# Performance work log

Hardware: AMD Instinct MI355X
Metric: run time of the kernel (lower is better)

Reference implementation:

```python
import jax, jax.numpy as jnp
import numpy as np

B, T, D = 2, 2048, 1024
H = 16
DH = D // H            # 64, per-head dim
C = 128                # d_kv_compress
ROPE_BASE = 10000.0


def _rope_cos_sin(t_len, d_head, dtype):
    # freqs: (T, d_head/2); emb = cat(freqs, freqs) -> (T, d_head)
    inv_freq = 1.0 / (ROPE_BASE ** (jnp.arange(0, d_head, 2, dtype=jnp.float32) / d_head))
    freqs = jnp.arange(t_len, dtype=jnp.float32)[:, None] * inv_freq[None, :]
    emb = jnp.concatenate([freqs, freqs], axis=-1)
    return jnp.cos(emb).astype(dtype), jnp.sin(emb).astype(dtype)


def _rotate_half(x):
    x1, x2 = jnp.split(x, 2, axis=-1)
    return jnp.concatenate([-x2, x1], axis=-1)


def _apply_rope(x, cos, sin):
    # x: (B,H,T,DH); cos/sin: (T,DH)
    return x * cos[None, None] + _rotate_half(x) * sin[None, None]


def setup_inputs() -> dict:
    key = jax.random.key(0)
    ks = jax.random.split(key, 12)
    s = 0.02
    return {
        "x": jax.random.normal(ks[0], (B, T, D), dtype=jnp.float32),
        "w_dk": jax.random.normal(ks[1], (D, C), dtype=jnp.float32) * s,
        "b_dk": jnp.zeros((C,), dtype=jnp.float32),
        "w_dv": jax.random.normal(ks[2], (D, C), dtype=jnp.float32) * s,
        "b_dv": jnp.zeros((C,), dtype=jnp.float32),
        "w_uk": jax.random.normal(ks[3], (C, D), dtype=jnp.float32) * s,
        "b_uk": jnp.zeros((D,), dtype=jnp.float32),
        "w_uv": jax.random.normal(ks[4], (C, D), dtype=jnp.float32) * s,
        "b_uv": jnp.zeros((D,), dtype=jnp.float32),
        "w_o": jax.random.normal(ks[5], (D, D), dtype=jnp.float32) * s,
        "b_o": jnp.zeros((D,), dtype=jnp.float32),
    }


def reference(x, w_dk, b_dk, w_dv, b_dv, w_uk, b_uk, w_uv, b_uv, w_o, b_o):
    Bx, Tx, Dx = x.shape
    # low-rank KV compression then up-projection
    c_k = x @ w_dk + b_dk                      # (B,T,C)
    c_v = x @ w_dv + b_dv                      # (B,T,C)
    k = c_k @ w_uk + b_uk                      # (B,T,D)
    v = c_v @ w_uv + b_uv                      # (B,T,D)

    def split_heads(t):  # (B,T,D) -> (B,H,T,DH)
        return t.reshape(Bx, Tx, H, DH).transpose(0, 2, 1, 3)

    q = split_heads(x)
    k = split_heads(k)
    v = split_heads(v)

    cos, sin = _rope_cos_sin(Tx, DH, x.dtype)
    q = _apply_rope(q, cos, sin)
    k = _apply_rope(k, cos, sin)

    scale = 1.0 / np.sqrt(DH)
    attn = jnp.einsum('bhid,bhjd->bhij', q, k) * scale
    attn = jax.nn.softmax(attn, axis=-1)
    out = jnp.einsum('bhij,bhjd->bhid', attn, v)   # (B,H,T,DH)
    out = out.transpose(0, 2, 1, 3).reshape(Bx, Tx, Dx)
    return out @ w_o + b_o
```

## Files before the change

### kernel.cpp

```cpp
#include <hip/hip_runtime.h>
#include <hip/hip_bf16.h>
#include <math.h>

constexpr int kB  = 2;
constexpr int kT  = 2048;
constexpr int kD  = 1024;
constexpr int kH  = 16;
constexpr int kDH = 64;
constexpr int kC  = 128;
constexpr int kM  = kB * kT;
constexpr int kBH = kB * kH;

#define LOG10000_OVER_32 0.28782313662425575f
#define QSCALE 0.1803368801111773f

typedef unsigned short ushort_t;
using short8 = __attribute__((ext_vector_type(8))) short;
using f32x4  = __attribute__((ext_vector_type(4))) float;

__device__ inline ushort_t f2bf(float f) {
    __hip_bfloat16 h = __float2bfloat16(f);
    return *reinterpret_cast<ushort_t*>(&h);
}

__device__ inline short8 cvt8(const float* p) {
    float4 f0 = *reinterpret_cast<const float4*>(p);
    float4 f1 = *reinterpret_cast<const float4*>(p + 4);
    short8 v;
    v[0] = (short)f2bf(f0.x); v[1] = (short)f2bf(f0.y);
    v[2] = (short)f2bf(f0.z); v[3] = (short)f2bf(f0.w);
    v[4] = (short)f2bf(f1.x); v[5] = (short)f2bf(f1.y);
    v[6] = (short)f2bf(f1.z); v[7] = (short)f2bf(f1.w);
    return v;
}

__global__ __launch_bounds__(256)
void wtrans(const float* __restrict__ w_dk, const float* __restrict__ w_dv,
            const float* __restrict__ w_uk, const float* __restrict__ w_uv,
            const float* __restrict__ w_o,
            ushort_t* __restrict__ dkT, ushort_t* __restrict__ dvT,
            ushort_t* __restrict__ ukT, ushort_t* __restrict__ uvT,
            ushort_t* __restrict__ oT, float2* __restrict__ tab) {
    if (blockIdx.z == 5) {
        int flat = blockIdx.y * 32 + blockIdx.x;
        if (flat >= kT / 8) return;
        int t = flat * 8 + (threadIdx.x >> 5);
        int i = threadIdx.x & 31;
        float inv_freq = expf(-(float)i * LOG10000_OVER_32);
        float s, c;
        sincosf((float)t * inv_freq, &s, &c);
        tab[t * 32 + i] = make_float2(c, s);
        return;
    }
    const float* src; ushort_t* dst; int R, C;
    switch (blockIdx.z) {
        case 0: src = w_dk; dst = dkT; R = kD; C = kC; break;
        case 1: src = w_dv; dst = dvT; R = kD; C = kC; break;
        case 2: src = w_uk; dst = ukT; R = kC; C = kD; break;
        case 3: src = w_uv; dst = uvT; R = kC; C = kD; break;
        default: src = w_o; dst = oT;  R = kD; C = kD; break;
    }
    int c0 = blockIdx.x * 32, r0 = blockIdx.y * 32;
    if (c0 >= C || r0 >= R) return;

    __shared__ float Tl[32][33];
    int tx = threadIdx.x & 31, ty = threadIdx.x >> 5;
#pragma unroll
    for (int i = 0; i < 4; ++i)
        Tl[ty + 8 * i][tx] = src[(size_t)(r0 + ty + 8 * i) * C + c0 + tx];
    __syncthreads();
#pragma unroll
    for (int i = 0; i < 4; ++i)
        dst[(size_t)(c0 + ty + 8 * i) * R + r0 + tx] = f2bf(Tl[tx][ty + 8 * i]);
}

template<bool AF32, int MODE0, int MODE1>
__global__ __launch_bounds__(256)
void gemm_mfma(const void* __restrict__ A0_, const void* __restrict__ A1_,
               const ushort_t* __restrict__ Wt0, const float* __restrict__ bias0, void* __restrict__ C0,
               const ushort_t* __restrict__ Wt1, const float* __restrict__ bias1, void* __restrict__ C1,
               const float2* __restrict__ tab, int M, int N, int K) {
    constexpr int LDT = 40;
    __shared__ __align__(16) ushort_t As[128 * LDT];
    __shared__ __align__(16) ushort_t Bs[128 * LDT];

    const void*     A    = blockIdx.z ? A1_ : A0_;
    const ushort_t* Wt   = blockIdx.z ? Wt1 : Wt0;
    const float*    bias = blockIdx.z ? bias1 : bias0;
    void*           Cc   = blockIdx.z ? C1 : C0;
    const int       mode = blockIdx.z ? MODE1 : MODE0;

    const int tid  = threadIdx.x;
    const int wave = tid >> 6, lane = tid & 63;
    const int g = lane >> 4, cl = lane & 15;
    const int m0 = blockIdx.y * 128, n0 = blockIdx.x * 128;
    const int wm = (wave >> 1) * 64, wn = (wave & 1) * 64;

    const int ar = tid >> 1;
    const int ac = (tid & 1) * 16;

    f32x4 acc[4][4] = {};

    for (int k0 = 0; k0 < K; k0 += 32) {
        if constexpr (AF32) {
            const float* Af = (const float*)A + (size_t)(m0 + ar) * K + k0 + ac;
            *reinterpret_cast<short8*>(&As[ar * LDT + ac])     = cvt8(Af);
            *reinterpret_cast<short8*>(&As[ar * LDT + ac + 8]) = cvt8(Af + 8);
        } else {
            const ushort_t* Ab = (const ushort_t*)A + (size_t)(m0 + ar) * K + k0 + ac;
            *reinterpret_cast<short8*>(&As[ar * LDT + ac])     = *reinterpret_cast<const short8*>(Ab);
            *reinterpret_cast<short8*>(&As[ar * LDT + ac + 8]) = *reinterpret_cast<const short8*>(Ab + 8);
        }
        {
            const ushort_t* Wb = Wt + (size_t)(n0 + ar) * K + k0 + ac;
            *reinterpret_cast<short8*>(&Bs[ar * LDT + ac])     = *reinterpret_cast<const short8*>(Wb);
            *reinterpret_cast<short8*>(&Bs[ar * LDT + ac + 8]) = *reinterpret_cast<const short8*>(Wb + 8);
        }
        __syncthreads();

        short8 a[4], b[4];
#pragma unroll
        for (int mi = 0; mi < 4; ++mi)
            a[mi] = *reinterpret_cast<const short8*>(&As[(wm + mi * 16 + cl) * LDT + g * 8]);
#pragma unroll
        for (int ni = 0; ni < 4; ++ni)
            b[ni] = *reinterpret_cast<const short8*>(&Bs[(wn + ni * 16 + cl) * LDT + g * 8]);
#pragma unroll
        for (int mi = 0; mi < 4; ++mi)
#pragma unroll
            for (int ni = 0; ni < 4; ++ni)
                acc[mi][ni] = __builtin_amdgcn_mfma_f32_16x16x32_bf16(a[mi], b[ni], acc[mi][ni], 0, 0, 0);
        __syncthreads();
    }

#pragma unroll
    for (int mi = 0; mi < 4; ++mi) {
        if (mode == 4) {
            const int h = (n0 + wn) >> 6;
#pragma unroll
            for (int r = 0; r < 4; ++r) {
                const int m = m0 + wm + mi * 16 + 4 * g + r;
                const int bb = m >> 11, t = m & (kT - 1);
                ushort_t* kp = (ushort_t*)Cc + (((size_t)bb * kH + h) * kT + t) * kDH;
#pragma unroll
                for (int pr = 0; pr < 2; ++pr) {
                    const int i = pr * 16 + cl;
                    float2 cs = tab[t * 32 + i];
                    float v1 = acc[mi][pr][r]     + bias[n0 + wn + pr * 16 + cl];
                    float v2 = acc[mi][pr + 2][r] + bias[n0 + wn + (pr + 2) * 16 + cl];
                    kp[i]      = f2bf(v1 * cs.x - v2 * cs.y);
                    kp[i + 32] = f2bf(v2 * cs.x + v1 * cs.y);
                }
            }
            continue;
        }
#pragma unroll
        for (int ni = 0; ni < 4; ++ni) {
            const int mb = m0 + wm + mi * 16 + 4 * g;
            const int nn = n0 + wn + ni * 16 + cl;
            const float bv = bias[nn];
            if (mode == 0) {
#pragma unroll
                for (int r = 0; r < 4; ++r)
                    ((float*)Cc)[(size_t)(mb + r) * N + nn] = acc[mi][ni][r] + bv;
            } else if (mode == 3) {
#pragma unroll
                for (int r = 0; r < 4; ++r)
                    ((ushort_t*)Cc)[(size_t)(mb + r) * N + nn] = f2bf(acc[mi][ni][r] + bv);
            } else {
                const int h = nn >> 6, d = nn & (kDH - 1);
                const int bb = mb >> 11, t0 = mb & (kT - 1);
                uint2 u;
                u.x = (unsigned int)f2bf(acc[mi][ni][0] + bv) | ((unsigned int)f2bf(acc[mi][ni][1] + bv) << 16);
                u.y = (unsigned int)f2bf(acc[mi][ni][2] + bv) | ((unsigned int)f2bf(acc[mi][ni][3] + bv) << 16);
                ushort_t* vt = (ushort_t*)Cc;
                *reinterpret_cast<uint2*>(&vt[(((size_t)bb * kH + h) * kDH + d) * kT + t0]) = u;
            }
        }
    }
}

__global__ __launch_bounds__(256)
void rope_split_q(const float* __restrict__ x, const float2* __restrict__ tab,
                  ushort_t* __restrict__ q_bf) {
    int idx = blockIdx.x * 256 + threadIdx.x;
    int i = idx & 31;
    int h = (idx >> 5) & (kH - 1);
    int t = (idx >> 9) & (kT - 1);
    int b = idx >> 20;

    const float* xp = x + ((size_t)(b * kT + t)) * kD + h * kDH;
    float x1 = xp[i];
    float x2 = xp[i + 32];
    float2 cs = tab[t * 32 + i];

    ushort_t* qp = q_bf + (((size_t)(b * kH + h)) * kT + t) * kDH;
    qp[i]      = f2bf((x1 * cs.x - x2 * cs.y) * QSCALE);
    qp[i + 32] = f2bf((x2 * cs.x + x1 * cs.y) * QSCALE);
}

__global__ __launch_bounds__(256)
void attn_mfma(const ushort_t* __restrict__ q_bf, const ushort_t* __restrict__ k_bf,
               const ushort_t* __restrict__ vt_bf, ushort_t* __restrict__ att_bf) {
    constexpr int LDK = 72;
    constexpr int LDV = 40;
    constexpr int LDP = 36;
    const int blk  = blockIdx.x;
    const int bh   = (blk & 7) * 4 + ((blk >> 3) & 3);
    const int qt   = blk >> 5;
    const int tid  = threadIdx.x;
    const int wave = tid >> 6;
    const int lane = tid & 63;
    const int g = lane >> 4, c = lane & 15;
    const int qbase = qt * 128 + wave * 32;

    __shared__ __align__(16) ushort_t Ks[32 * LDK];
    __shared__ __align__(16) ushort_t Vs[64 * LDV];
    __shared__ __align__(16) ushort_t P_lds[4][32 * LDP];
    ushort_t* P = P_lds[wave];

    const ushort_t* qp = q_bf + ((size_t)bh * kT + qbase) * kDH;
    short8 qa[2][2];
#pragma unroll
    for (int qi = 0; qi < 2; ++qi)
#pragma unroll
        for (int f = 0; f < 2; ++f)
            qa[qi][f] = *reinterpret_cast<const short8*>(qp + (size_t)(qi * 16 + c) * kDH + f * 32 + g * 8);

    const ushort_t* kb = k_bf + (size_t)bh * kT * kDH;
    const ushort_t* vb = vt_bf + (size_t)bh * kDH * kT;

    const int kr_ = tid >> 3, kc_ = (tid & 7) * 8;
    const int vr_ = tid >> 2, vc_ = (tid & 3) * 8;

    f32x4 acc[2][4] = {};
    float lsum[2][4] = {};

    for (int kt = 0; kt < kT; kt += 32) {
        *reinterpret_cast<short8*>(&Ks[kr_ * LDK + kc_]) =
            *reinterpret_cast<const short8*>(&kb[(size_t)(kt + kr_) * kDH + kc_]);
        *reinterpret_cast<short8*>(&Vs[vr_ * LDV + vc_]) =
            *reinterpret_cast<const short8*>(&vb[(size_t)vr_ * kT + kt + vc_]);
        __syncthreads();

        short8 kf[2][2];
#pragma unroll
        for (int kj = 0; kj < 2; ++kj)
#pragma unroll
            for (int f = 0; f < 2; ++f)
                kf[kj][f] = *reinterpret_cast<const short8*>(&Ks[(kj * 16 + c) * LDK + f * 32 + g * 8]);

        f32x4 z = {0.f, 0.f, 0.f, 0.f};
        f32x4 s[2][2];
#pragma unroll
        for (int qi = 0; qi < 2; ++qi)
#pragma unroll
            for (int kj = 0; kj < 2; ++kj) {
                s[qi][kj] = __builtin_amdgcn_mfma_f32_16x16x32_bf16(qa[qi][0], kf[kj][0], z, 0, 0, 0);
                s[qi][kj] = __builtin_amdgcn_mfma_f32_16x16x32_bf16(qa[qi][1], kf[kj][1], s[qi][kj], 0, 0, 0);
            }

#pragma unroll
        for (int qi = 0; qi < 2; ++qi)
#pragma unroll
            for (int kj = 0; kj < 2; ++kj)
#pragma unroll
                for (int r = 0; r < 4; ++r) {
                    float p = exp2f(s[qi][kj][r]);
                    lsum[qi][r] += p;
                    P[(qi * 16 + 4 * g + r) * LDP + kj * 16 + c] = f2bf(p);
                }

        short8 pa[2];
#pragma unroll
        for (int qi = 0; qi < 2; ++qi)
            pa[qi] = *reinterpret_cast<const short8*>(&P[(qi * 16 + c) * LDP + g * 8]);

        short8 vf[4];
#pragma unroll
        for (int n = 0; n < 4; ++n)
            vf[n] = *reinterpret_cast<const short8*>(&Vs[(16 * n + c) * LDV + g * 8]);
#pragma unroll
        for (int qi = 0; qi < 2; ++qi)
#pragma unroll
            for (int n = 0; n < 4; ++n)
                acc[qi][n] = __builtin_amdgcn_mfma_f32_16x16x32_bf16(pa[qi], vf[n], acc[qi][n], 0, 0, 0);
        __syncthreads();
    }

#pragma unroll
    for (int off = 1; off < 16; off <<= 1)
#pragma unroll
        for (int qi = 0; qi < 2; ++qi)
#pragma unroll
            for (int r = 0; r < 4; ++r)
                lsum[qi][r] += __shfl_xor(lsum[qi][r], off, 64);

    const int b = bh >> 4, h = bh & (kH - 1);
#pragma unroll
    for (int qi = 0; qi < 2; ++qi)
#pragma unroll
        for (int r = 0; r < 4; ++r) {
            float inv_l = 1.0f / lsum[qi][r];
            size_t row = (size_t)(b * kT + qbase + qi * 16 + 4 * g + r) * kD + h * kDH;
#pragma unroll
            for (int n = 0; n < 4; ++n)
                att_bf[row + 16 * n + c] = f2bf(acc[qi][n][r] * inv_l);
        }
}

extern "C" void kernel_launch(void* const* d_in, const int* in_sizes, int n_in,
                              void* d_out, int out_size, void* d_ws, size_t ws_size,
                              hipStream_t stream) {
    const float* x    = (const float*)d_in[0];
    const float* w_dk = (const float*)d_in[1];
    const float* b_dk = (const float*)d_in[2];
    const float* w_dv = (const float*)d_in[3];
    const float* b_dv = (const float*)d_in[4];
    const float* w_uk = (const float*)d_in[5];
    const float* b_uk = (const float*)d_in[6];
    const float* w_uv = (const float*)d_in[7];
    const float* b_uv = (const float*)d_in[8];
    const float* w_o  = (const float*)d_in[9];
    const float* b_o  = (const float*)d_in[10];
    float* out = (float*)d_out;

    char* w = (char*)d_ws;
    ushort_t* q_bf   = (ushort_t*)w;  w += (size_t)kM * kD * 2;
    ushort_t* k_bf   = (ushort_t*)w;  w += (size_t)kM * kD * 2;
    ushort_t* vt_bf  = (ushort_t*)w;  w += (size_t)kM * kD * 2;
    ushort_t* att_bf = (ushort_t*)w;  w += (size_t)kM * kD * 2;
    ushort_t* ckbf   = (ushort_t*)w;  w += (size_t)kM * kC * 2;
    ushort_t* cvbf   = (ushort_t*)w;  w += (size_t)kM * kC * 2;
    ushort_t* dkT    = (ushort_t*)w;  w += (size_t)kC * kD * 2;
    ushort_t* dvT    = (ushort_t*)w;  w += (size_t)kC * kD * 2;
    ushort_t* ukT    = (ushort_t*)w;  w += (size_t)kD * kC * 2;
    ushort_t* uvT    = (ushort_t*)w;  w += (size_t)kD * kC * 2;
    ushort_t* oT     = (ushort_t*)w;  w += (size_t)kD * kD * 2;
    float2*   tab    = (float2*)w;    w += (size_t)kT * 32 * 8;

    dim3 blk(256);

    wtrans<<<dim3(32, 32, 6), blk, 0, stream>>>(w_dk, w_dv, w_uk, w_uv, w_o,
                                                dkT, dvT, ukT, uvT, oT, tab);

    gemm_mfma<true, 3, 3><<<dim3(kC / 128, kM / 128, 2), blk, 0, stream>>>(
        x, x, dkT, b_dk, ckbf, dvT, b_dv, cvbf, nullptr, kM, kC, kD);

    gemm_mfma<false, 4, 2><<<dim3(kD / 128, kM / 128, 2), blk, 0, stream>>>(
        ckbf, cvbf, ukT, b_uk, k_bf, uvT, b_uv, vt_bf, tab, kM, kD, kC);

    rope_split_q<<<(kB * kT * kH * 32) / 256, blk, 0, stream>>>(x, tab, q_bf);

    attn_mfma<<<dim3(kT / 128 * kBH), blk, 0, stream>>>(q_bf, k_bf, vt_bf, att_bf);

    gemm_mfma<false, 0, 0><<<dim3(kD / 128, kM / 128, 1), blk, 0, stream>>>(
        att_bf, att_bf, oT, b_o, out, oT, b_o, out, nullptr, kM, kD, kD);
}
```

Measured before the change: 266.0 us.

## Fuse Q RoPE into attention, double-buffer K/V, add 128x64 GEMM for small-N

Removes the separate rope_split_q kernel and q_bf buffer by computing rotated, scaled Q from x directly in the attention kernel. Attention now uses 16 query rows per wave with 64-row blocks, doubling grid size, and double-buffers K/V tiles in LDS with register prefetch so there is one barrier per step. A new 128x64-tile GEMM is used for the down-projection and output projection to raise block count. The up-projection GEMM is specialized to bf16 A only. Trade-off: less Q reuse per block and more K/V traffic per query.

```diff
diff --git a/kernel.cpp b/kernel.cpp
--- a/kernel.cpp
+++ b/kernel.cpp
@@ -74,9 +74,9 @@
         dst[(size_t)(c0 + ty + 8 * i) * R + r0 + tx] = f2bf(Tl[tx][ty + 8 * i]);
 }
 
-template<bool AF32, int MODE0, int MODE1>
+template<int MODE0, int MODE1>
 __global__ __launch_bounds__(256)
-void gemm_mfma(const void* __restrict__ A0_, const void* __restrict__ A1_,
+void gemm_mfma(const ushort_t* __restrict__ A0_, const ushort_t* __restrict__ A1_,
                const ushort_t* __restrict__ Wt0, const float* __restrict__ bias0, void* __restrict__ C0,
                const ushort_t* __restrict__ Wt1, const float* __restrict__ bias1, void* __restrict__ C1,
                const float2* __restrict__ tab, int M, int N, int K) {
@@ -84,7 +84,7 @@
     __shared__ __align__(16) ushort_t As[128 * LDT];
     __shared__ __align__(16) ushort_t Bs[128 * LDT];
 
-    const void*     A    = blockIdx.z ? A1_ : A0_;
+    const ushort_t* A    = blockIdx.z ? A1_ : A0_;
     const ushort_t* Wt   = blockIdx.z ? Wt1 : Wt0;
     const float*    bias = blockIdx.z ? bias1 : bias0;
     void*           Cc   = blockIdx.z ? C1 : C0;
@@ -100,6 +100,95 @@
     const int ac = (tid & 1) * 16;
 
     f32x4 acc[4][4] = {};
+
+    for (int k0 = 0; k0 < K; k0 += 32) {
+        {
+            const ushort_t* Ab = A + (size_t)(m0 + ar) * K + k0 + ac;
+            *reinterpret_cast<short8*>(&As[ar * LDT + ac])     = *reinterpret_cast<const short8*>(Ab);
+            *reinterpret_cast<short8*>(&As[ar * LDT + ac + 8]) = *reinterpret_cast<const short8*>(Ab + 8);
+            const ushort_t* Wb = Wt + (size_t)(n0 + ar) * K + k0 + ac;
+            *reinterpret_cast<short8*>(&Bs[ar * LDT + ac])     = *reinterpret_cast<const short8*>(Wb);
+            *reinterpret_cast<short8*>(&Bs[ar * LDT + ac + 8]) = *reinterpret_cast<const short8*>(Wb + 8);
+        }
+        __syncthreads();
+
+        short8 a[4], b[4];
+#pragma unroll
+        for (int mi = 0; mi < 4; ++mi)
+            a[mi] = *reinterpret_cast<const short8*>(&As[(wm + mi * 16 + cl) * LDT + g * 8]);
+#pragma unroll
+        for (int ni = 0; ni < 4; ++ni)
+            b[ni] = *reinterpret_cast<const short8*>(&Bs[(wn + ni * 16 + cl) * LDT + g * 8]);
+#pragma unroll
+        for (int mi = 0; mi < 4; ++mi)
+#pragma unroll
+            for (int ni = 0; ni < 4; ++ni)
+                acc[mi][ni] = __builtin_amdgcn_mfma_f32_16x16x32_bf16(a[mi], b[ni], acc[mi][ni], 0, 0, 0);
+        __syncthreads();
+    }
+
+#pragma unroll
+    for (int mi = 0; mi < 4; ++mi) {
+        if (mode == 4) {
+            const int h = (n0 + wn) >> 6;
+#pragma unroll
+            for (int r = 0; r < 4; ++r) {
+                const int m = m0 + wm + mi * 16 + 4 * g + r;
+                const int bb = m >> 11, t = m & (kT - 1);
+                ushort_t* kp = (ushort_t*)Cc + (((size_t)bb * kH + h) * kT + t) * kDH;
+#pragma unroll
+                for (int pr = 0; pr < 2; ++pr) {
+                    const int i = pr * 16 + cl;
+                    float2 cs = tab[t * 32 + i];
+                    float v1 = acc[mi][pr][r]     + bias[n0 + wn + pr * 16 + cl];
+                    float v2 = acc[mi][pr + 2][r] + bias[n0 + wn + (pr + 2) * 16 + cl];
+                    kp[i]      = f2bf(v1 * cs.x - v2 * cs.y);
+                    kp[i + 32] = f2bf(v2 * cs.x + v1 * cs.y);
+                }
+            }
+        } else {
+#pragma unroll
+            for (int ni = 0; ni < 4; ++ni) {
+                const int mb = m0 + wm + mi * 16 + 4 * g;
+                const int nn = n0 + wn + ni * 16 + cl;
+                const float bv = bias[nn];
+                const int h = nn >> 6, d = nn & (kDH - 1);
+                const int bb = mb >> 11, t0 = mb & (kT - 1);
+                uint2 u;
+                u.x = (unsigned int)f2bf(acc[mi][ni][0] + bv) | ((unsigned int)f2bf(acc[mi][ni][1] + bv) << 16);
+                u.y = (unsigned int)f2bf(acc[mi][ni][2] + bv) | ((unsigned int)f2bf(acc[mi][ni][3] + bv) << 16);
+                ushort_t* vt = (ushort_t*)Cc;
+                *reinterpret_cast<uint2*>(&vt[(((size_t)bb * kH + h) * kDH + d) * kT + t0]) = u;
+            }
+        }
+    }
+}
+
+template<bool AF32, int MODE>
+__global__ __launch_bounds__(256)
+void gemm64(const void* __restrict__ A0_, const void* __restrict__ A1_,
+            const ushort_t* __restrict__ Wt0, const float* __restrict__ bias0, void* __restrict__ C0,
+            const ushort_t* __restrict__ Wt1, const float* __restrict__ bias1, void* __restrict__ C1,
+            int M, int N, int K) {
+    constexpr int LDT = 40;
+    __shared__ __align__(16) ushort_t As[128 * LDT];
+    __shared__ __align__(16) ushort_t Bs[64 * LDT];
+
+    const void*     A    = blockIdx.z ? A1_ : A0_;
+    const ushort_t* Wt   = blockIdx.z ? Wt1 : Wt0;
+    const float*    bias = blockIdx.z ? bias1 : bias0;
+    void*           Cc   = blockIdx.z ? C1 : C0;
+
+    const int tid  = threadIdx.x;
+    const int wave = tid >> 6, lane = tid & 63;
+    const int g = lane >> 4, cl = lane & 15;
+    const int m0 = blockIdx.y * 128, n0 = blockIdx.x * 64;
+    const int wm = (wave >> 1) * 64, wn = (wave & 1) * 32;
+
+    const int ar = tid >> 1, ac = (tid & 1) * 16;
+    const int br = tid >> 2, bc = (tid & 3) * 8;
+
+    f32x4 acc[4][2] = {};
 
     for (int k0 = 0; k0 < K; k0 += 32) {
         if constexpr (AF32) {
@@ -111,97 +200,48 @@
             *reinterpret_cast<short8*>(&As[ar * LDT + ac])     = *reinterpret_cast<const short8*>(Ab);
             *reinterpret_cast<short8*>(&As[ar * LDT + ac + 8]) = *reinterpret_cast<const short8*>(Ab + 8);
         }
-        {
-            const ushort_t* Wb = Wt + (size_t)(n0 + ar) * K + k0 + ac;
-            *reinterpret_cast<short8*>(&Bs[ar * LDT + ac])     = *reinterpret_cast<const short8*>(Wb);
-            *reinterpret_cast<short8*>(&Bs[ar * LDT + ac + 8]) = *reinterpret_cast<const short8*>(Wb + 8);
-        }
+        *reinterpret_cast<short8*>(&Bs[br * LDT + bc]) =
+            *reinterpret_cast<const short8*>(Wt + (size_t)(n0 + br) * K + k0 + bc);
         __syncthreads();
 
-        short8 a[4], b[4];
+        short8 a[4], b[2];
 #pragma unroll
         for (int mi = 0; mi < 4; ++mi)
             a[mi] = *reinterpret_cast<const short8*>(&As[(wm + mi * 16 + cl) * LDT + g * 8]);
 #pragma unroll
-        for (int ni = 0; ni < 4; ++ni)
+        for (int ni = 0; ni < 2; ++ni)
             b[ni] = *reinterpret_cast<const short8*>(&Bs[(wn + ni * 16 + cl) * LDT + g * 8]);
 #pragma unroll
         for (int mi = 0; mi < 4; ++mi)
 #pragma unroll
-            for (int ni = 0; ni < 4; ++ni)
+            for (int ni = 0; ni < 2; ++ni)
                 acc[mi][ni] = __builtin_amdgcn_mfma_f32_16x16x32_bf16(a[mi], b[ni], acc[mi][ni], 0, 0, 0);
         __syncthreads();
     }
 
 #pragma unroll
-    for (int mi = 0; mi < 4; ++mi) {
-        if (mode == 4) {
-            const int h = (n0 + wn) >> 6;
-#pragma unroll
-            for (int r = 0; r < 4; ++r) {
-                const int m = m0 + wm + mi * 16 + 4 * g + r;
-                const int bb = m >> 11, t = m & (kT - 1);
-                ushort_t* kp = (ushort_t*)Cc + (((size_t)bb * kH + h) * kT + t) * kDH;
-#pragma unroll
-                for (int pr = 0; pr < 2; ++pr) {
-                    const int i = pr * 16 + cl;
-                    float2 cs = tab[t * 32 + i];
-                    float v1 = acc[mi][pr][r]     + bias[n0 + wn + pr * 16 + cl];
-                    float v2 = acc[mi][pr + 2][r] + bias[n0 + wn + (pr + 2) * 16 + cl];
-                    kp[i]      = f2bf(v1 * cs.x - v2 * cs.y);
-                    kp[i + 32] = f2bf(v2 * cs.x + v1 * cs.y);
-                }
-            }
-            continue;
-        }
-#pragma unroll
-        for (int ni = 0; ni < 4; ++ni) {
+    for (int mi = 0; mi < 4; ++mi)
+#pragma unroll
+        for (int ni = 0; ni < 2; ++ni) {
             const int mb = m0 + wm + mi * 16 + 4 * g;
             const int nn = n0 + wn + ni * 16 + cl;
             const float bv = bias[nn];
-            if (mode == 0) {
+            if constexpr (MODE == 0) {
 #pragma unroll
                 for (int r = 0; r < 4; ++r)
                     ((float*)Cc)[(size_t)(mb + r) * N + nn] = acc[mi][ni][r] + bv;
-            } else if (mode == 3) {
+            } else {
 #pragma unroll
                 for (int r = 0; r < 4; ++r)
                     ((ushort_t*)Cc)[(size_t)(mb + r) * N + nn] = f2bf(acc[mi][ni][r] + bv);
-            } else {
-                const int h = nn >> 6, d = nn & (kDH - 1);
-                const int bb = mb >> 11, t0 = mb & (kT - 1);
-                uint2 u;
-                u.x = (unsigned int)f2bf(acc[mi][ni][0] + bv) | ((unsigned int)f2bf(acc[mi][ni][1] + bv) << 16);
-                u.y = (unsigned int)f2bf(acc[mi][ni][2] + bv) | ((unsigned int)f2bf(acc[mi][ni][3] + bv) << 16);
-                ushort_t* vt = (ushort_t*)Cc;
-                *reinterpret_cast<uint2*>(&vt[(((size_t)bb * kH + h) * kDH + d) * kT + t0]) = u;
             }
         }
-    }
 }
 
 __global__ __launch_bounds__(256)
-void rope_split_q(const float* __restrict__ x, const float2* __restrict__ tab,
-                  ushort_t* __restrict__ q_bf) {
-    int idx = blockIdx.x * 256 + threadIdx.x;
-    int i = idx & 31;
-    int h = (idx >> 5) & (kH - 1);
-    int t = (idx >> 9) & (kT - 1);
-    int b = idx >> 20;
-
-    const float* xp = x + ((size_t)(b * kT + t)) * kD + h * kDH;
-    float x1 = xp[i];
-    float x2 = xp[i + 32];
-    float2 cs = tab[t * 32 + i];
-
-    ushort_t* qp = q_bf + (((size_t)(b * kH + h)) * kT + t) * kDH;
-    qp[i]      = f2bf((x1 * cs.x - x2 * cs.y) * QSCALE);
-    qp[i + 32] = f2bf((x2 * cs.x + x1 * cs.y) * QSCALE);
-}
-
-__global__ __launch_bounds__(256)
-void attn_mfma(const ushort_t* __restrict__ q_bf, const ushort_t* __restrict__ k_bf,
-               const ushort_t* __restrict__ vt_bf, ushort_t* __restrict__ att_bf) {
+void attn_mfma(const float* __restrict__ x, const float2* __restrict__ tab,
+               const ushort_t* __restrict__ k_bf, const ushort_t* __restrict__ vt_bf,
+               ushort_t* __restrict__ att_bf) {
     constexpr int LDK = 72;
     constexpr int LDV = 40;
     constexpr int LDP = 36;
@@ -209,23 +249,35 @@
     const int bh   = (blk & 7) * 4 + ((blk >> 3) & 3);
     const int qt   = blk >> 5;
     const int tid  = threadIdx.x;
-    const int wave = tid >> 6;
-    const int lane = tid & 63;
+    const int wave = tid >> 6, lane = tid & 63;
     const int g = lane >> 4, c = lane & 15;
-    const int qbase = qt * 128 + wave * 32;
-
-    __shared__ __align__(16) ushort_t Ks[32 * LDK];
-    __shared__ __align__(16) ushort_t Vs[64 * LDV];
-    __shared__ __align__(16) ushort_t P_lds[4][32 * LDP];
+    const int qbase = qt * 64 + wave * 16;
+    const int b = bh >> 4, h = bh & (kH - 1);
+
+    __shared__ __align__(16) ushort_t Ks[2][32 * LDK];
+    __shared__ __align__(16) ushort_t Vs[2][64 * LDV];
+    __shared__ __align__(16) ushort_t P_lds[4][16 * LDP];
     ushort_t* P = P_lds[wave];
 
-    const ushort_t* qp = q_bf + ((size_t)bh * kT + qbase) * kDH;
-    short8 qa[2][2];
-#pragma unroll
-    for (int qi = 0; qi < 2; ++qi)
-#pragma unroll
-        for (int f = 0; f < 2; ++f)
-            qa[qi][f] = *reinterpret_cast<const short8*>(qp + (size_t)(qi * 16 + c) * kDH + f * 32 + g * 8);
+    short8 qa0, qa1;
+    {
+        const int t = qbase + c;
+        const float* xp = x + ((size_t)(b * kT + t)) * kD + h * kDH + g * 8;
+        float xa[8], xb[8]; float2 cs[8];
+        *reinterpret_cast<float4*>(&xa[0]) = *reinterpret_cast<const float4*>(xp);
+        *reinterpret_cast<float4*>(&xa[4]) = *reinterpret_cast<const float4*>(xp + 4);
+        *reinterpret_cast<float4*>(&xb[0]) = *reinterpret_cast<const float4*>(xp + 32);
+        *reinterpret_cast<float4*>(&xb[4]) = *reinterpret_cast<const float4*>(xp + 36);
+        const float2* tp = tab + (size_t)t * 32 + g * 8;
+#pragma unroll
+        for (int j = 0; j < 8; j += 2)
+            *reinterpret_cast<float4*>(&cs[j]) = *reinterpret_cast<const float4*>(tp + j);
+#pragma unroll
+        for (int j = 0; j < 8; ++j) {
+            qa0[j] = (short)f2bf((xa[j] * cs[j].x - xb[j] * cs[j].y) * QSCALE);
+            qa1[j] = (short)f2bf((xb[j] * cs[j].x + xa[j] * cs[j].y) * QSCALE);
+        }
+    }
 
     const ushort_t* kb = k_bf + (size_t)bh * kT * kDH;
     const ushort_t* vb = vt_bf + (size_t)bh * kDH * kT;
@@ -233,80 +285,78 @@
     const int kr_ = tid >> 3, kc_ = (tid & 7) * 8;
     const int vr_ = tid >> 2, vc_ = (tid & 3) * 8;
 
-    f32x4 acc[2][4] = {};
-    float lsum[2][4] = {};
+    {
+        short8 kreg = *reinterpret_cast<const short8*>(&kb[(size_t)kr_ * kDH + kc_]);
+        short8 vreg = *reinterpret_cast<const short8*>(&vb[(size_t)vr_ * kT + vc_]);
+        *reinterpret_cast<short8*>(&Ks[0][kr_ * LDK + kc_]) = kreg;
+        *reinterpret_cast<short8*>(&Vs[0][vr_ * LDV + vc_]) = vreg;
+    }
+    __syncthreads();
+
+    f32x4 acc[4] = {};
+    float lsum[4] = {};
 
     for (int kt = 0; kt < kT; kt += 32) {
-        *reinterpret_cast<short8*>(&Ks[kr_ * LDK + kc_]) =
-            *reinterpret_cast<const short8*>(&kb[(size_t)(kt + kr_) * kDH + kc_]);
-        *reinterpret_cast<short8*>(&Vs[vr_ * LDV + vc_]) =
-            *reinterpret_cast<const short8*>(&vb[(size_t)vr_ * kT + kt + vc_]);
+        const int cur = (kt >> 5) & 1;
+        short8 kreg, vreg;
+        const bool more = (kt + 32) < kT;
+        if (more) {
+            kreg = *reinterpret_cast<const short8*>(&kb[(size_t)(kt + 32 + kr_) * kDH + kc_]);
+            vreg = *reinterpret_cast<const short8*>(&vb[(size_t)vr_ * kT + kt + 32 + vc_]);
+        }
+
+        short8 kf[2][2];
+#pragma unroll
+        for (int kj = 0; kj < 2; ++kj)
+#pragma unroll
+            for (int f = 0; f < 2; ++f)
+                kf[kj][f] = *reinterpret_cast<const short8*>(&Ks[cur][(kj * 16 + c) * LDK + f * 32 + g * 8]);
+
+        f32x4 z = {0.f, 0.f, 0.f, 0.f};
+        f32x4 s0 = __builtin_amdgcn_mfma_f32_16x16x32_bf16(qa0, kf[0][0], z, 0, 0, 0);
+        s0 = __builtin_amdgcn_mfma_f32_16x16x32_bf16(qa1, kf[0][1], s0, 0, 0, 0);
+        f32x4 s1 = __builtin_amdgcn_mfma_f32_16x16x32_bf16(qa0, kf[1][0], z, 0, 0, 0);
+        s1 = __builtin_amdgcn_mfma_f32_16x16x32_bf16(qa1, kf[1][1], s1, 0, 0, 0);
+
+#pragma unroll
+        for (int r = 0; r < 4; ++r) {
+            float p0 = exp2f(s0[r]);
+            float p1 = exp2f(s1[r]);
+            lsum[r] += p0 + p1;
+            P[(4 * g + r) * LDP + c]      = f2bf(p0);
+            P[(4 * g + r) * LDP + 16 + c] = f2bf(p1);
+        }
+        short8 pa = *reinterpret_cast<const short8*>(&P[c * LDP + g * 8]);
+
+        short8 vf[4];
+#pragma unroll
+        for (int n = 0; n < 4; ++n)
+            vf[n] = *reinterpret_cast<const short8*>(&Vs[cur][(16 * n + c) * LDV + g * 8]);
+#pragma unroll
+        for (int n = 0; n < 4; ++n)
+            acc[n] = __builtin_amdgcn_mfma_f32_16x16x32_bf16(pa, vf[n], acc[n], 0, 0, 0);
+
+        if (more) {
+            *reinterpret_cast<short8*>(&Ks[cur ^ 1][kr_ * LDK + kc_]) = kreg;
+            *reinterpret_cast<short8*>(&Vs[cur ^ 1][vr_ * LDV + vc_]) = vreg;
+        }
         __syncthreads();
-
-        short8 kf[2][2];
-#pragma unroll
-        for (int kj = 0; kj < 2; ++kj)
-#pragma unroll
-            for (int f = 0; f < 2; ++f)
-                kf[kj][f] = *reinterpret_cast<const short8*>(&Ks[(kj * 16 + c) * LDK + f * 32 + g * 8]);
-
-        f32x4 z = {0.f, 0.f, 0.f, 0.f};
-        f32x4 s[2][2];
-#pragma unroll
-        for (int qi = 0; qi < 2; ++qi)
-#pragma unroll
-            for (int kj = 0; kj < 2; ++kj) {
-                s[qi][kj] = __builtin_amdgcn_mfma_f32_16x16x32_bf16(qa[qi][0], kf[kj][0], z, 0, 0, 0);
-                s[qi][kj] = __builtin_amdgcn_mfma_f32_16x16x32_bf16(qa[qi][1], kf[kj][1], s[qi][kj], 0, 0, 0);
-            }
-
-#pragma unroll
-        for (int qi = 0; qi < 2; ++qi)
-#pragma unroll
-            for (int kj = 0; kj < 2; ++kj)
-#pragma unroll
-                for (int r = 0; r < 4; ++r) {
-                    float p = exp2f(s[qi][kj][r]);
-                    lsum[qi][r] += p;
-                    P[(qi * 16 + 4 * g + r) * LDP + kj * 16 + c] = f2bf(p);
-                }
-
-        short8 pa[2];
-#pragma unroll
-        for (int qi = 0; qi < 2; ++qi)
-            pa[qi] = *reinterpret_cast<const short8*>(&P[(qi * 16 + c) * LDP + g * 8]);
-
-        short8 vf[4];
+    }
+
+#pragma unroll
+    for (int off = 1; off < 16; off <<= 1)
+#pragma unroll
+        for (int r = 0; r < 4; ++r)
+            lsum[r] += __shfl_xor(lsum[r], off, 64);
+
+#pragma unroll
+    for (int r = 0; r < 4; ++r) {
+        float inv_l = 1.0f / lsum[r];
+        size_t row = (size_t)(b * kT + qbase + 4 * g + r) * kD + h * kDH;
 #pragma unroll
         for (int n = 0; n < 4; ++n)
-            vf[n] = *reinterpret_cast<const short8*>(&Vs[(16 * n + c) * LDV + g * 8]);
-#pragma unroll
-        for (int qi = 0; qi < 2; ++qi)
-#pragma unroll
-            for (int n = 0; n < 4; ++n)
-                acc[qi][n] = __builtin_amdgcn_mfma_f32_16x16x32_bf16(pa[qi], vf[n], acc[qi][n], 0, 0, 0);
-        __syncthreads();
-    }
-
-#pragma unroll
-    for (int off = 1; off < 16; off <<= 1)
-#pragma unroll
-        for (int qi = 0; qi < 2; ++qi)
-#pragma unroll
-            for (int r = 0; r < 4; ++r)
-                lsum[qi][r] += __shfl_xor(lsum[qi][r], off, 64);
-
-    const int b = bh >> 4, h = bh & (kH - 1);
-#pragma unroll
-    for (int qi = 0; qi < 2; ++qi)
-#pragma unroll
-        for (int r = 0; r < 4; ++r) {
-            float inv_l = 1.0f / lsum[qi][r];
-            size_t row = (size_t)(b * kT + qbase + qi * 16 + 4 * g + r) * kD + h * kDH;
-#pragma unroll
-            for (int n = 0; n < 4; ++n)
-                att_bf[row + 16 * n + c] = f2bf(acc[qi][n][r] * inv_l);
-        }
+            att_bf[row + 16 * n + c] = f2bf(acc[n][r] * inv_l);
+    }
 }
 
 extern "C" void kernel_launch(void* const* d_in, const int* in_sizes, int n_in,
@@ -326,7 +376,6 @@
     float* out = (float*)d_out;
 
     char* w = (char*)d_ws;
-    ushort_t* q_bf   = (ushort_t*)w;  w += (size_t)kM * kD * 2;
     ushort_t* k_bf   = (ushort_t*)w;  w += (size_t)kM * kD * 2;
     ushort_t* vt_bf  = (ushort_t*)w;  w += (size_t)kM * kD * 2;
     ushort_t* att_bf = (ushort_t*)w;  w += (size_t)kM * kD * 2;
@@ -344,16 +393,14 @@
     wtrans<<<dim3(32, 32, 6), blk, 0, stream>>>(w_dk, w_dv, w_uk, w_uv, w_o,
                                                 dkT, dvT, ukT, uvT, oT, tab);
 
-    gemm_mfma<true, 3, 3><<<dim3(kC / 128, kM / 128, 2), blk, 0, stream>>>(
-        x, x, dkT, b_dk, ckbf, dvT, b_dv, cvbf, nullptr, kM, kC, kD);
-
-    gemm_mfma<false, 4, 2><<<dim3(kD / 128, kM / 128, 2), blk, 0, stream>>>(
+    gemm64<true, 3><<<dim3(kC / 64, kM / 128, 2), blk, 0, stream>>>(
+        x, x, dkT, b_dk, ckbf, dvT, b_dv, cvbf, kM, kC, kD);
+
+    gemm_mfma<4, 2><<<dim3(kD / 128, kM / 128, 2), blk, 0, stream>>>(
         ckbf, cvbf, ukT, b_uk, k_bf, uvT, b_uv, vt_bf, tab, kM, kD, kC);
 
-    rope_split_q<<<(kB * kT * kH * 32) / 256, blk, 0, stream>>>(x, tab, q_bf);
-
-    attn_mfma<<<dim3(kT / 128 * kBH), blk, 0, stream>>>(q_bf, k_bf, vt_bf, att_bf);
-
-    gemm_mfma<false, 0, 0><<<dim3(kD / 128, kM / 128, 1), blk, 0, stream>>>(
-        att_bf, att_bf, oT, b_o, out, oT, b_o, out, nullptr, kM, kD, kD);
-}
+    attn_mfma<<<dim3(kT / 64 * kBH), blk, 0, stream>>>(x, tab, k_bf, vt_bf, att_bf);
+
+    gemm64<false, 0><<<dim3(kD / 64, kM / 128, 1), blk, 0, stream>>>(
+        att_bf, att_bf, oT, b_o, out, oT, b_o, out, kM, kD, kD);
+}
```

Measured after the change: 249.0 us. 1.07x faster.
